# Optimization experiments

Measured on AMD Instinct MI355X. Metric: run time of the kernel, lower is better.

The kernel has to match this reference:

```python
import jax, jax.numpy as jnp
import numpy as np

T, B, H, W, CIN = 20, 16, 128, 128, 2
CH, OUT = 64, 10
BETA, THR = 0.9, 1.0


def spike(u):
    # Heaviside fire (surrogate grad only matters in bwd module)
    return (u > 0.0).astype(u.dtype)


def setup_inputs() -> dict:
    key = jax.random.key(0)
    k0, k1, k2 = jax.random.split(key, 3)
    x_seq = jax.random.normal(k0, (T, B, H, W, CIN), jnp.float32)
    w_conv = jax.random.normal(k1, (3, 3, CIN, CH), jnp.float32) * (1.0 / np.sqrt(9 * CIN))
    b_conv = jnp.zeros((CH,), jnp.float32)
    w_head = jax.random.normal(k2, (CH, OUT), jnp.float32) * (1.0 / np.sqrt(CH))
    b_head = jnp.zeros((OUT,), jnp.float32)
    return {"x_seq": x_seq, "w_conv": w_conv, "b_conv": b_conv,
            "w_head": w_head, "b_head": b_head}


def reference(x_seq, w_conv, b_conv, w_head, b_head):
    # temporal frame differences: [T-1, B, H, W, CIN]
    flow = x_seq[1:] - x_seq[:-1]
    t, b, h, w, c = flow.shape
    # conv is carry-independent: batch it over (time*batch) in one call
    u = jax.lax.conv_general_dilated(
        flow.reshape(t * b, h, w, c), w_conv,
        window_strides=(1, 1), padding='SAME',
        dimension_numbers=('NHWC', 'HWIO', 'NHWC')) + b_conv
    u = u.reshape(t, b, h, w, CH)  # [T-1, B, H, W, CH]

    def step(V, u_t):
        # LIF: leaky integrate, fire, soft reset
        V = BETA * V + u_t
        s = spike(V - THR)
        V = V - s * THR
        y = jnp.mean(s, axis=(1, 2)) @ w_head + b_head  # [B, OUT]
        return V, (y, jnp.mean(s))

    V0 = jnp.zeros((b, h, w, CH), u.dtype)
    _, (logits_seq, sr_seq) = jax.lax.scan(step, V0, u)
    readout = jnp.mean(logits_seq, axis=0)  # 'mean' readout
    return readout, logits_seq, jnp.asarray([jnp.mean(sr_seq)])
```

## Files before the change

kernel.cpp:

```cpp
#include <hip/hip_runtime.h>
#include <hip/hip_bf16.h>

#define TT   20
#define TS   19
#define BB   16
#define HH   128
#define WW   128
#define CINN 2
#define CHN  64
#define NOUT 10
#define BETA 0.9f
#define INVB (1.0f / BETA)

#define NCHUNK 5
#define NPB    128
#define SR_IDX (BB*NOUT + TS*BB*NOUT)

#define PPD      132
#define ROWB     (PPD*4)
#define PROWS    129
#define PLANE_B  (PROWS*ROWB)
#define FRAME_B  (2*PLANE_B)
#define FLOW_B   ((size_t)BB*TS*FRAME_B)
#define SLACK_B  528
#define CNT_OFF4 ((size_t)(FLOW_B + SLACK_B) / 4)
#define CNT_B    ((size_t)BB*NCHUNK*NPB*CHN*4)
#define WS_NEED  (FLOW_B + SLACK_B + CNT_B)

#define LROW  20

typedef __attribute__((ext_vector_type(8))) short short8;
typedef __attribute__((ext_vector_type(4))) float float4v;
typedef __attribute__((ext_vector_type(4))) int   int4v;
typedef unsigned uint4v_t __attribute__((ext_vector_type(4)));
typedef uint4v_t __attribute__((aligned(4))) uint4vu;
typedef unsigned uint2v_t __attribute__((ext_vector_type(2)));
typedef uint2v_t __attribute__((aligned(4))) uint2vu;

__device__ __forceinline__ unsigned rne16(float f) {
    unsigned u = __float_as_uint(f);
    return (u + 0x7fffu + ((u >> 16) & 1u)) >> 16;
}
__device__ __forceinline__ float b2f(unsigned us) { return __uint_as_float(us << 16); }
__device__ __forceinline__ unsigned rndb(float f) {
    unsigned u = __float_as_uint(f);
    return u + 0x7fffu + ((u >> 16) & 1u);
}
__device__ __forceinline__ void pack2(float d0, float d1, unsigned &hi, unsigned &lo) {
    unsigned r0 = rndb(d0), r1 = rndb(d1);
    hi = __builtin_amdgcn_perm(r1, r0, 0x07060302u);
    float e0 = d0 - __uint_as_float(r0 & 0xffff0000u);
    float e1 = d1 - __uint_as_float(r1 & 0xffff0000u);
    lo = __builtin_amdgcn_perm(rndb(e1), rndb(e0), 0x07060302u);
}

__global__ __launch_bounds__(256) void flow_pack(const float* __restrict__ x,
                                                 unsigned* __restrict__ wsf) {
    const int bx  = blockIdx.x;
    const int b   = blockIdx.y;
    const int tid = threadIdx.x;
    const int row = (bx << 2) + (tid >> 6);
    const int p0  = (tid & 63) << 1;

    const int TSTR = BB * HH * WW / 2;
    const float4* xr = (const float4*)x + ((b * HH + row) * WW + p0) / 2;
    char* fb = (char*)wsf + (size_t)b * TS * FRAME_B;
    const unsigned off = (unsigned)(row * PPD + p0 + 1) * 4u;

    float4 cur = xr[0];
    float4 nxt = xr[TSTR];
    float ct = 1.f;
#pragma unroll 1
    for (int t = 0; t < TS; ++t) {
        float4 fut = nxt;
        if (t + 2 <= TS) fut = xr[(t + 2) * TSTR];
        float d0 = (nxt.x - cur.x) * ct, d1 = (nxt.y - cur.y) * ct;
        float d2 = (nxt.z - cur.z) * ct, d3 = (nxt.w - cur.w) * ct;
        unsigned h0, l0, h1, l1;
        pack2(d0, d1, h0, l0);
        pack2(d2, d3, h1, l1);
        uint2v_t hv = {h0, h1}, lv = {l0, l1};
        *(uint2vu*)(fb + off) = hv;
        *(uint2vu*)(fb + PLANE_B + off) = lv;
        if ((tid & 63) < 8) {
            int c  = tid & 7;
            int pl = c >> 2;
            int pp = (c & 3) == 0 ? 0 : 128 + (c & 3);
            *(unsigned*)(fb + pl * PLANE_B + (row * PPD + pp) * 4) = 0u;
        }
        if (bx == 0) {
            for (int d = tid; d < 2 * PPD; d += 256) {
                int pl = d >= PPD, pp = d - pl * PPD;
                *(unsigned*)(fb + pl * PLANE_B + (128 * PPD + pp) * 4) = 0u;
            }
        }
        cur = nxt; nxt = fut;
        fb += FRAME_B; ct *= INVB;
    }
    if (bx == 0 && b == 0 && tid < PPD)
        *((unsigned*)((char*)wsf + FLOW_B) + tid) = 0u;
}

__global__ __launch_bounds__(256, 3) void lif_fast(const char* __restrict__ flow,
                                                   const float* __restrict__ w_conv,
                                                   const float* __restrict__ b_conv,
                                                   int* __restrict__ cw,
                                                   float* __restrict__ out) {
    __shared__ int lds_cnt[NCHUNK][CHN];

    const int tid  = threadIdx.x;
    const int lane = tid & 63;
    const int wv   = __builtin_amdgcn_readfirstlane(tid >> 6);
    const int bx   = blockIdx.x;
    const int r0   = blockIdx.y << 1;
    const int bz   = blockIdx.z;
    const int q    = lane >> 4;
    const int col  = lane & 15;
    const int x0   = (bx << 6) + (wv << 4);
    const int qsh  = q << 3;

    if (bx == 0 && blockIdx.y == 0 && bz == 0) {
        if (tid < BB * NOUT) out[tid] = 0.f;
        else if (tid == BB * NOUT) out[SR_IDX] = 0.f;
    }
    if (tid < NCHUNK * CHN - 256) ((int*)lds_cnt)[256 + tid] = 0;
    ((int*)lds_cnt)[tid] = 0;
    __syncthreads();

    const int rq  = (q < 3) ? q : 0;
    const int yA0 = r0 - 1 + rq, yA1 = yA0 + 1;
    const int ym0 = ((unsigned)yA0 < (unsigned)HH) ? yA0 : 128;
    const int ym1 = ((unsigned)yA1 < (unsigned)HH) ? yA1 : 128;
    const unsigned offH0 = (unsigned)(ym0 * ROWB + (x0 + col) * 4);
    const unsigned offH1 = (unsigned)(ym1 * ROWB + (x0 + col) * 4);

    short8 Bh[4], Bl[4];
#pragma unroll
    for (int cg = 0; cg < 4; ++cg) {
        int hi_i[4] = {0, 0, 0, 0}, lo_i[4] = {0, 0, 0, 0};
        if (q < 3) {
#pragma unroll
            for (int j = 0; j < 6; ++j) {
                float w = w_conv[((q * 3 + (j >> 1)) * 2 + (j & 1)) * CHN + cg * 16 + col];
                unsigned hs = rne16(w);
                unsigned ls = rne16(w - b2f(hs));
                hi_i[j >> 1] |= (int)(hs << (16 * (j & 1)));
                lo_i[j >> 1] |= (int)(ls << (16 * (j & 1)));
            }
        }
        int4v hv = {hi_i[0], hi_i[1], hi_i[2], hi_i[3]};
        int4v lv = {lo_i[0], lo_i[1], lo_i[2], lo_i[3]};
        Bh[cg] = __builtin_bit_cast(short8, hv);
        Bl[cg] = __builtin_bit_cast(short8, lv);
    }

    float nb[4];
#pragma unroll
    for (int cg = 0; cg < 4; ++cg) nb[cg] = -b_conv[cg * 16 + col];

    float4v W0[4], W1[4];
#pragma unroll
    for (int cg = 0; cg < 4; ++cg) {
        W0[cg] = (float4v){0.f, 0.f, 0.f, 0.f};
        W1[cg] = (float4v){0.f, 0.f, 0.f, 0.f};
    }

    float ct = 1.0f, S = 1.0f;
    int pendA = 0, pendB = 0;
    unsigned cur = 0;

    const char* fp = flow + (size_t)bz * TS * FRAME_B;
    uint4vu eH0 = *(const uint4vu*)(fp + offH0);
    uint4vu eH1 = *(const uint4vu*)(fp + offH1);
    uint4vu eL0 = *(const uint4vu*)(fp + PLANE_B + offH0);
    uint4vu eL1 = *(const uint4vu*)(fp + PLANE_B + offH1);
    fp += FRAME_B;
    uint4vu oH0, oH1, oL0, oL1;

#define STEP(T_, CH0, CH1, CL0, CL1, NH0, NH1, NL0, NL1, DPOS, DODEF, DOFLUSH, CK, DOLOAD) do { \
    int cp1_ = 0, sh2_ = 0;                                                     \
    if (DODEF) { cp1_ = pendA + pendB; sh2_ = __shfl_xor(cp1_, 32); }           \
    if (DOLOAD) {                                                               \
        NH0 = *(const uint4vu*)(fp + offH0);                                    \
        NH1 = *(const uint4vu*)(fp + offH1);                                    \
        NL0 = *(const uint4vu*)(fp + PLANE_B + offH0);                          \
        NL1 = *(const uint4vu*)(fp + PLANE_B + offH1);                          \
        fp += FRAME_B;                                                          \
    }                                                                           \
    float ctn = ct * INVB;                                                      \
    short8 A0h = __builtin_bit_cast(short8, CH0);                               \
    short8 A1h = __builtin_bit_cast(short8, CH1);                               \
    short8 A0l = __builtin_bit_cast(short8, CL0);                               \
    short8 A1l = __builtin_bit_cast(short8, CL1);                               \
    __builtin_amdgcn_s_setprio(1);                                              \
    _Pragma("unroll")                                                           \
    for (int cg = 0; cg < 4; ++cg) {                                            \
        W0[cg] = __builtin_amdgcn_mfma_f32_16x16x32_bf16(A0h, Bh[cg], W0[cg], 0, 0, 0); \
        W1[cg] = __builtin_amdgcn_mfma_f32_16x16x32_bf16(A1h, Bh[cg], W1[cg], 0, 0, 0); \
    }                                                                           \
    _Pragma("unroll")                                                           \
    for (int cg = 0; cg < 4; ++cg) {                                            \
        W0[cg] = __builtin_amdgcn_mfma_f32_16x16x32_bf16(A0l, Bh[cg], W0[cg], 0, 0, 0); \
        W1[cg] = __builtin_amdgcn_mfma_f32_16x16x32_bf16(A1l, Bh[cg], W1[cg], 0, 0, 0); \
    }                                                                           \
    _Pragma("unroll")                                                           \
    for (int cg = 0; cg < 4; ++cg) {                                            \
        W0[cg] = __builtin_amdgcn_mfma_f32_16x16x32_bf16(A0h, Bl[cg], W0[cg], 0, 0, 0); \
        W1[cg] = __builtin_amdgcn_mfma_f32_16x16x32_bf16(A1h, Bl[cg], W1[cg], 0, 0, 0); \
    }                                                                           \
    __builtin_amdgcn_s_setprio(0);                                              \
    if (DODEF) {                                                                \
        unsigned cnt_ = ((unsigned)(cp1_ + sh2_) >> qsh) & 255u;                \
        cur |= cnt_ << (8 * (DPOS));                                            \
        if (DOFLUSH) { atomicAdd(&lds_cnt[CK][lane], (int)cur); cur = 0u; }     \
    }                                                                           \
    int cpack = 0;                                                              \
    _Pragma("unroll")                                                           \
    for (int cg = 0; cg < 4; ++cg) {                                            \
        float thr = fmaf(nb[cg], S, ct);                                        \
        float4v w0 = W0[cg], w1 = W1[cg];                                       \
        int c = 0;                                                              \
        _Pragma("unroll")                                                       \
        for (int r = 0; r < 4; ++r) {                                           \
            float v0 = w0[r]; bool s0 = v0 > thr;                               \
            w0[r] = s0 ? (v0 - ct) : v0; c += s0;                               \
            float v1 = w1[r]; bool s1 = v1 > thr;                               \
            w1[r] = s1 ? (v1 - ct) : v1; c += s1;                               \
        }                                                                       \
        W0[cg] = w0; W1[cg] = w1;                                               \
        cpack |= c << (8 * cg);                                                 \
    }                                                                           \
    pendA = cpack;                                                              \
    pendB = __shfl_xor(cpack, 16);                                              \
    ct = ctn; S += ctn;                                                         \
} while (0)

#pragma unroll 1
    for (int c = 0; c < 4; ++c) {
        STEP(4 * c + 0, eH0, eH1, eL0, eL1, oH0, oH1, oL0, oL1, 3, (c > 0), (c > 0), (c - 1), 1);
        STEP(4 * c + 1, oH0, oH1, oL0, oL1, eH0, eH1, eL0, eL1, 0, 1, 0, 0, 1);
        STEP(4 * c + 2, eH0, eH1, eL0, eL1, oH0, oH1, oL0, oL1, 1, 1, 0, 0, 1);
        STEP(4 * c + 3, oH0, oH1, oL0, oL1, eH0, eH1, eL0, eL1, 2, 1, 0, 0, 1);
    }
    STEP(16, eH0, eH1, eL0, eL1, oH0, oH1, oL0, oL1, 3, 1, 1, 3, 1);
    STEP(17, oH0, oH1, oL0, oL1, eH0, eH1, eL0, eL1, 0, 1, 0, 0, 1);
    STEP(18, eH0, eH1, eL0, eL1, oH0, oH1, oL0, oL1, 1, 1, 0, 0, 0);
#undef STEP

    {
        int cp1 = pendA + pendB;
        int cp2 = cp1 + __shfl_xor(cp1, 32);
        unsigned cnt = ((unsigned)cp2 >> qsh) & 255u;
        cur |= cnt << 16;
        atomicAdd(&lds_cnt[4][lane], (int)cur);
    }
    __syncthreads();

    {
        const int pb = (blockIdx.y << 1) | bx;
        const int k0 = tid >> 6, ch = tid & 63;
        cw[((bz * NCHUNK + k0) * NPB + pb) * CHN + ch] = lds_cnt[k0][ch];
        if (tid < CHN)
            cw[((bz * NCHUNK + 4) * NPB + pb) * CHN + tid] = lds_cnt[4][tid];
    }
}

__global__ __launch_bounds__(256, 4) void lif_main(const float* __restrict__ x,
                                                   const float* __restrict__ w_conv,
                                                   const float* __restrict__ b_conv,
                                                   int* __restrict__ ws,
                                                   float* __restrict__ out) {
    __shared__ unsigned lds[4][2][2][4 * LROW];
    __shared__ int lds_cnt[NCHUNK][CHN];

    const float2* xp2 = (const float2*)x;
    const int FRAME2  = BB * HH * WW;

    const int tid  = threadIdx.x;
    const int lane = tid & 63;
    const int wv   = __builtin_amdgcn_readfirstlane(tid >> 6);
    const int bx   = blockIdx.x;
    const int r0   = blockIdx.y << 1;
    const int bz   = blockIdx.z;
    const int q    = lane >> 4;
    const int col  = lane & 15;
    const int x0   = (bx << 6) + (wv << 4);
    const int qsh  = q << 3;

    if (bx == 0 && blockIdx.y == 0 && bz == 0) {
        if (tid < BB * NOUT) out[tid] = 0.f;
        else if (tid == BB * NOUT) out[SR_IDX] = 0.f;
    }
    if (tid < NCHUNK * CHN - 256) ((int*)lds_cnt)[256 + tid] = 0;
    ((int*)lds_cnt)[tid] = 0;
    __syncthreads();

    const int  row0 = lane / 18, dx0 = lane - row0 * 18;
    const int  y0s  = r0 - 1 + row0;
    const int  px0s = x0 - 1 + dx0;
    const bool val0 = ((unsigned)y0s < (unsigned)HH) && ((unsigned)px0s < (unsigned)WW);
    const int  off0 = val0 ? (y0s * WW + px0s) : 0;
    const int  ls0  = row0 * LROW + dx0;

    const bool act1 = (lane < 8);
    const int  y1s  = r0 + 2;
    const int  px1s = x0 - 1 + 10 + lane;
    const bool val1 = act1 && ((unsigned)y1s < (unsigned)HH) && ((unsigned)px1s < (unsigned)WW);
    const int  off1 = val1 ? (y1s * WW + px1s) : 0;
    const int  ls1  = 3 * LROW + 10 + lane;

    const int rq  = (q < 3) ? q : 0;
    const int rdb = rq * LROW + col;

    short8 Bh[4], Bl[4];
#pragma unroll
    for (int cg = 0; cg < 4; ++cg) {
        int hi_i[4] = {0, 0, 0, 0}, lo_i[4] = {0, 0, 0, 0};
        if (q < 3) {
#pragma unroll
            for (int j = 0; j < 6; ++j) {
                float w = w_conv[((q * 3 + (j >> 1)) * 2 + (j & 1)) * CHN + cg * 16 + col];
                unsigned hs = rne16(w);
                unsigned ls = rne16(w - b2f(hs));
                hi_i[j >> 1] |= (int)(hs << (16 * (j & 1)));
                lo_i[j >> 1] |= (int)(ls << (16 * (j & 1)));
            }
        }
        int4v hv = {hi_i[0], hi_i[1], hi_i[2], hi_i[3]};
        int4v lv = {lo_i[0], lo_i[1], lo_i[2], lo_i[3]};
        Bh[cg] = __builtin_bit_cast(short8, hv);
        Bl[cg] = __builtin_bit_cast(short8, lv);
    }

    float nb[4];
#pragma unroll
    for (int cg = 0; cg < 4; ++cg) nb[cg] = -b_conv[cg * 16 + col];

    float4v W0[4], W1[4];
#pragma unroll
    for (int cg = 0; cg < 4; ++cg) {
        W0[cg] = (float4v){0.f, 0.f, 0.f, 0.f};
        W1[cg] = (float4v){0.f, 0.f, 0.f, 0.f};
    }

    float ct = 1.0f, S = 1.0f;
    int pendA = 0, pendB = 0;
    unsigned cur = 0;

    float2 ra_0 = {0.f, 0.f}, rb_0 = {0.f, 0.f}, rc_0 = {0.f, 0.f};
    float2 ra_1 = {0.f, 0.f}, rb_1 = {0.f, 0.f}, rc_1 = {0.f, 0.f};
    const float2* xb = xp2 + bz * HH * WW;
    if (val0) { rb_0 = xb[off0]; ra_0 = xb[FRAME2 + off0]; rc_0 = xb[2 * FRAME2 + off0]; }
    if (val1) { rb_1 = xb[off1]; ra_1 = xb[FRAME2 + off1]; rc_1 = xb[2 * FRAME2 + off1]; }
    {
        unsigned* hiW = &lds[wv][0][0][0];
        unsigned* loW = &lds[wv][0][1][0];
        {
            float d0 = (ra_0.x - rb_0.x), d1 = (ra_0.y - rb_0.y);
            unsigned hw, lw; pack2(d0, d1, hw, lw);
            hiW[ls0] = hw; loW[ls0] = lw;
        }
        if (act1) {
            float d0 = (ra_1.x - rb_1.x), d1 = (ra_1.y - rb_1.y);
            unsigned hw, lw; pack2(d0, d1, hw, lw);
            hiW[ls1] = hw; loW[ls1] = lw;
        }
        rb_0 = ra_0; ra_0 = rc_0;
        rb_1 = ra_1; ra_1 = rc_1;
        if (val0) rc_0 = xb[3 * FRAME2 + off0];
        if (val1) rc_1 = xb[3 * FRAME2 + off1];
    }
    const float2* xn = xb + 4 * FRAME2;

#define STEP(T_, CURB, NXTB, DPOS, DODEF, DOFLUSH, CK, DOSTAGE, DOPREF) do {    \
    const unsigned* hiR = &lds[wv][CURB][0][0] + rdb;                           \
    const unsigned* loR = &lds[wv][CURB][1][0] + rdb;                           \
    unsigned h0 = hiR[0], h1 = hiR[1], h2 = hiR[2];                             \
    unsigned h3 = hiR[LROW], h4 = hiR[LROW + 1], h5 = hiR[LROW + 2];            \
    unsigned l0 = loR[0], l1 = loR[1], l2 = loR[2];                             \
    unsigned l3 = loR[LROW], l4 = loR[LROW + 1], l5 = loR[LROW + 2];            \
    int cp1_ = 0, sh2_ = 0;                                                     \
    if (DODEF) { cp1_ = pendA + pendB; sh2_ = __shfl_xor(cp1_, 32); }           \
    float ctn = ct * INVB;                                                      \
    if (DOSTAGE) {                                                              \
        unsigned* hiW = &lds[wv][NXTB][0][0];                                   \
        unsigned* loW = &lds[wv][NXTB][1][0];                                   \
        {                                                                       \
            float d0 = (ra_0.x - rb_0.x) * ctn;                                 \
            float d1 = (ra_0.y - rb_0.y) * ctn;                                 \
            unsigned hw, lw; pack2(d0, d1, hw, lw);                             \
            hiW[ls0] = hw; loW[ls0] = lw;                                       \
        }                                                                       \
        if (act1) {                                                             \
            float d0 = (ra_1.x - rb_1.x) * ctn;                                 \
            float d1 = (ra_1.y - rb_1.y) * ctn;                                 \
            unsigned hw, lw; pack2(d0, d1, hw, lw);                             \
            hiW[ls1] = hw; loW[ls1] = lw;                                       \
        }                                                                       \
        rb_0 = ra_0; ra_0 = rc_0;                                               \
        rb_1 = ra_1; ra_1 = rc_1;                                               \
        if (DOPREF) {                                                           \
            if (val0) rc_0 = xn[off0];                                          \
            if (val1) rc_1 = xn[off1];                                          \
            xn += FRAME2;                                                       \
        }                                                                       \
    }                                                                           \
    int4v a0h = {(int)h0, (int)h1, (int)h2, (int)h0};                           \
    int4v a0l = {(int)l0, (int)l1, (int)l2, (int)l0};                           \
    int4v a1h = {(int)h3, (int)h4, (int)h5, (int)h3};                           \
    int4v a1l = {(int)l3, (int)l4, (int)l5, (int)l3};                           \
    short8 A0h = __builtin_bit_cast(short8, a0h);                               \
    short8 A0l = __builtin_bit_cast(short8, a0l);                               \
    short8 A1h = __builtin_bit_cast(short8, a1h);                               \
    short8 A1l = __builtin_bit_cast(short8, a1l);                               \
    __builtin_amdgcn_s_setprio(1);                                              \
    _Pragma("unroll")                                                           \
    for (int cg = 0; cg < 4; ++cg) {                                            \
        W0[cg] = __builtin_amdgcn_mfma_f32_16x16x32_bf16(A0h, Bh[cg], W0[cg], 0, 0, 0); \
        W1[cg] = __builtin_amdgcn_mfma_f32_16x16x32_bf16(A1h, Bh[cg], W1[cg], 0, 0, 0); \
    }                                                                           \
    _Pragma("unroll")                                                           \
    for (int cg = 0; cg < 4; ++cg) {                                            \
        W0[cg] = __builtin_amdgcn_mfma_f32_16x16x32_bf16(A0l, Bh[cg], W0[cg], 0, 0, 0); \
        W1[cg] = __builtin_amdgcn_mfma_f32_16x16x32_bf16(A1l, Bh[cg], W1[cg], 0, 0, 0); \
    }                                                                           \
    _Pragma("unroll")                                                           \
    for (int cg = 0; cg < 4; ++cg) {                                            \
        W0[cg] = __builtin_amdgcn_mfma_f32_16x16x32_bf16(A0h, Bl[cg], W0[cg], 0, 0, 0); \
        W1[cg] = __builtin_amdgcn_mfma_f32_16x16x32_bf16(A1h, Bl[cg], W1[cg], 0, 0, 0); \
    }                                                                           \
    __builtin_amdgcn_s_setprio(0);                                              \
    if (DODEF) {                                                                \
        unsigned cnt_ = ((unsigned)(cp1_ + sh2_) >> qsh) & 255u;                \
        cur |= cnt_ << (8 * (DPOS));                                            \
        if (DOFLUSH) { atomicAdd(&lds_cnt[CK][lane], (int)cur); cur = 0u; }     \
    }                                                                           \
    int cpack = 0;                                                              \
    _Pragma("unroll")                                                           \
    for (int cg = 0; cg < 4; ++cg) {                                            \
        float thr = fmaf(nb[cg], S, ct);                                        \
        float4v w0 = W0[cg], w1 = W1[cg];                                       \
        int c = 0;                                                              \
        _Pragma("unroll")                                                       \
        for (int r = 0; r < 4; ++r) {                                           \
            float v0 = w0[r]; bool s0 = v0 > thr;                               \
            w0[r] = s0 ? (v0 - ct) : v0; c += s0;                               \
            float v1 = w1[r]; bool s1 = v1 > thr;                               \
            w1[r] = s1 ? (v1 - ct) : v1; c += s1;                               \
        }                                                                       \
        W0[cg] = w0; W1[cg] = w1;                                               \
        cpack |= c << (8 * cg);                                                 \
    }                                                                           \
    pendA = cpack;                                                              \
    pendB = __shfl_xor(cpack, 16);                                              \
    ct = ctn; S += ctn;                                                         \
} while (0)

#pragma unroll 1
    for (int c = 0; c < 4; ++c) {
        STEP(4 * c + 0, 0, 1, 3, (c > 0), (c > 0), (c - 1), 1, 1);
        STEP(4 * c + 1, 1, 0, 0, 1, 0, 0, 1, 1);
        STEP(4 * c + 2, 0, 1, 1, 1, 0, 0, 1, 1);
        STEP(4 * c + 3, 1, 0, 2, 1, 0, 0, 1, 1);
    }
    STEP(16, 0, 1, 3, 1, 1, 3, 1, 0);
    STEP(17, 1, 0, 0, 1, 0, 0, 1, 0);
    STEP(18, 0, 1, 1, 1, 0, 0, 0, 0);
#undef STEP

    {
        int cp1 = pendA + pendB;
        int cp2 = cp1 + __shfl_xor(cp1, 32);
        unsigned cnt = ((unsigned)cp2 >> qsh) & 255u;
        cur |= cnt << 16;
        atomicAdd(&lds_cnt[4][lane], (int)cur);
    }
    __syncthreads();

    {
        const int pb = (blockIdx.y << 1) | bx;
        const int k0 = tid >> 6, ch = tid & 63;
        ws[((bz * NCHUNK + k0) * NPB + pb) * CHN + ch] = lds_cnt[k0][ch];
        if (tid < CHN)
            ws[((bz * NCHUNK + 4) * NPB + pb) * CHN + tid] = lds_cnt[4][tid];
    }
}

__global__ __launch_bounds__(64) void head_kernel(const int* __restrict__ cw,
                                                  const float* __restrict__ w_head,
                                                  const float* __restrict__ b_head,
                                                  float* __restrict__ out) {
    const int t = blockIdx.x, b = blockIdx.y, ch = threadIdx.x;
    const int k = t >> 2, sh = (t & 3) << 3;
    const int* base = cw + ((b * NCHUNK + k) * NPB) * CHN + ch;

    int cnt = 0;
#pragma unroll 8
    for (int p = 0; p < NPB; ++p) cnt += (base[p * CHN] >> sh) & 255;

    const float s = (float)cnt * (1.f / (HH * WW));
    float acc[NOUT];
#pragma unroll
    for (int o = 0; o < NOUT; ++o) acc[o] = s * w_head[ch * NOUT + o];
    float tt = (float)cnt;
#pragma unroll
    for (int off = 32; off > 0; off >>= 1) {
#pragma unroll
        for (int o = 0; o < NOUT; ++o) acc[o] += __shfl_down(acc[o], off);
        tt += __shfl_down(tt, off);
    }
    if (ch == 0) {
#pragma unroll
        for (int o = 0; o < NOUT; ++o) {
            float lg = acc[o] + b_head[o];
            out[BB * NOUT + (t * BB + b) * NOUT + o] = lg;
            atomicAdd(&out[b * NOUT + o], lg * (1.f / TS));
        }
        atomicAdd(&out[SR_IDX], tt * (1.f / ((float)TS * BB * HH * WW * CHN)));
    }
}

extern "C" void kernel_launch(void* const* d_in, const int* in_sizes, int n_in,
                              void* d_out, int out_size, void* d_ws, size_t ws_size,
                              hipStream_t stream) {
    (void)in_sizes; (void)n_in; (void)out_size;
    const float* x      = (const float*)d_in[0];
    const float* w_conv = (const float*)d_in[1];
    const float* b_conv = (const float*)d_in[2];
    const float* w_head = (const float*)d_in[3];
    const float* b_head = (const float*)d_in[4];
    float* out = (float*)d_out;

    if (ws_size >= WS_NEED) {
        unsigned* wsf = (unsigned*)d_ws;
        int* cw = (int*)d_ws + CNT_OFF4;
        flow_pack<<<dim3(32, BB), 256, 0, stream>>>(x, wsf);
        lif_fast<<<dim3(2, HH / 2, BB), 256, 0, stream>>>((const char*)d_ws, w_conv, b_conv, cw, out);
        head_kernel<<<dim3(TS, BB), 64, 0, stream>>>(cw, w_head, b_head, out);
    } else {
        int* cw = (int*)d_ws;
        lif_main<<<dim3(2, HH / 2, BB), 256, 0, stream>>>(x, w_conv, b_conv, cw, out);
        head_kernel<<<dim3(TS, BB), 64, 0, stream>>>(cw, w_head, b_head, out);
    }
}
```

Measured before the change: 167.4 us.

## Switch LIF conv MFMA from 16x16x32 to 32x32x16 tiles and raise occupancy

Result: slower. 171.8 us (+2.7%).

```diff
diff --git a/kernel.cpp b/kernel.cpp
--- a/kernel.cpp
+++ b/kernel.cpp
@@ -31,6 +31,7 @@
 
 typedef __attribute__((ext_vector_type(8))) short short8;
 typedef __attribute__((ext_vector_type(4))) float float4v;
+typedef __attribute__((ext_vector_type(16))) float floatv16;
 typedef __attribute__((ext_vector_type(4))) int   int4v;
 typedef unsigned uint4v_t __attribute__((ext_vector_type(4)));
 typedef uint4v_t __attribute__((aligned(4))) uint4vu;
@@ -101,7 +102,7 @@
         *((unsigned*)((char*)wsf + FLOW_B) + tid) = 0u;
 }
 
-__global__ __launch_bounds__(256, 3) void lif_fast(const char* __restrict__ flow,
+__global__ __launch_bounds__(256, 4) void lif_fast(const char* __restrict__ flow,
                                                    const float* __restrict__ w_conv,
                                                    const float* __restrict__ b_conv,
                                                    int* __restrict__ cw,
@@ -114,10 +115,9 @@
     const int bx   = blockIdx.x;
     const int r0   = blockIdx.y << 1;
     const int bz   = blockIdx.z;
-    const int q    = lane >> 4;
-    const int col  = lane & 15;
+    const int h    = lane >> 5;
+    const int colB = lane & 31;
     const int x0   = (bx << 6) + (wv << 4);
-    const int qsh  = q << 3;
 
     if (bx == 0 && blockIdx.y == 0 && bz == 0) {
         if (tid < BB * NOUT) out[tid] = 0.f;
@@ -127,131 +127,125 @@
     ((int*)lds_cnt)[tid] = 0;
     __syncthreads();
 
-    const int rq  = (q < 3) ? q : 0;
-    const int yA0 = r0 - 1 + rq, yA1 = yA0 + 1;
-    const int ym0 = ((unsigned)yA0 < (unsigned)HH) ? yA0 : 128;
-    const int ym1 = ((unsigned)yA1 < (unsigned)HH) ? yA1 : 128;
-    const unsigned offH0 = (unsigned)(ym0 * ROWB + (x0 + col) * 4);
-    const unsigned offH1 = (unsigned)(ym1 * ROWB + (x0 + col) * 4);
-
-    short8 Bh[4], Bl[4];
-#pragma unroll
-    for (int cg = 0; cg < 4; ++cg) {
-        int hi_i[4] = {0, 0, 0, 0}, lo_i[4] = {0, 0, 0, 0};
-        if (q < 3) {
-#pragma unroll
-            for (int j = 0; j < 6; ++j) {
-                float w = w_conv[((q * 3 + (j >> 1)) * 2 + (j & 1)) * CHN + cg * 16 + col];
-                unsigned hs = rne16(w);
-                unsigned ls = rne16(w - b2f(hs));
-                hi_i[j >> 1] |= (int)(hs << (16 * (j & 1)));
-                lo_i[j >> 1] |= (int)(ls << (16 * (j & 1)));
+    const int rimg = r0 + ((lane >> 4) & 1);
+    const int xpx  = x0 + (lane & 15);
+    const int ya   = rimg - 1 + h;
+    const int yb   = rimg + 1;
+    const int yam  = ((unsigned)ya < (unsigned)HH) ? ya : 128;
+    const int ybm  = ((unsigned)yb < (unsigned)HH) ? yb : 128;
+    const unsigned offQ0 = (unsigned)(yam * ROWB + xpx * 4);
+    const unsigned offQ1 = (unsigned)(ybm * ROWB + xpx * 4);
+
+    short8 Bh[2][2], Bl[2][2];
+#pragma unroll
+    for (int t = 0; t < 2; ++t) {
+#pragma unroll
+        for (int m = 0; m < 2; ++m) {
+            const int q = 2 * m + h;
+            int hi_i[4] = {0, 0, 0, 0}, lo_i[4] = {0, 0, 0, 0};
+            if (q < 3) {
+#pragma unroll
+                for (int e = 0; e < 6; ++e) {
+                    float w = w_conv[((q * 3 + (e >> 1)) * 2 + (e & 1)) * CHN + t * 32 + colB];
+                    unsigned hs = rne16(w);
+                    unsigned ls = rne16(w - b2f(hs));
+                    hi_i[e >> 1] |= (int)(hs << (16 * (e & 1)));
+                    lo_i[e >> 1] |= (int)(ls << (16 * (e & 1)));
+                }
             }
-        }
-        int4v hv = {hi_i[0], hi_i[1], hi_i[2], hi_i[3]};
-        int4v lv = {lo_i[0], lo_i[1], lo_i[2], lo_i[3]};
-        Bh[cg] = __builtin_bit_cast(short8, hv);
-        Bl[cg] = __builtin_bit_cast(short8, lv);
-    }
-
-    float nb[4];
-#pragma unroll
-    for (int cg = 0; cg < 4; ++cg) nb[cg] = -b_conv[cg * 16 + col];
-
-    float4v W0[4], W1[4];
-#pragma unroll
-    for (int cg = 0; cg < 4; ++cg) {
-        W0[cg] = (float4v){0.f, 0.f, 0.f, 0.f};
-        W1[cg] = (float4v){0.f, 0.f, 0.f, 0.f};
-    }
+            int4v hv = {hi_i[0], hi_i[1], hi_i[2], hi_i[3]};
+            int4v lv = {lo_i[0], lo_i[1], lo_i[2], lo_i[3]};
+            Bh[t][m] = __builtin_bit_cast(short8, hv);
+            Bl[t][m] = __builtin_bit_cast(short8, lv);
+        }
+    }
+
+    const float nb0 = -b_conv[colB];
+    const float nb1 = -b_conv[32 + colB];
+
+    floatv16 W0 = {0.f,0.f,0.f,0.f,0.f,0.f,0.f,0.f,0.f,0.f,0.f,0.f,0.f,0.f,0.f,0.f};
+    floatv16 W1 = {0.f,0.f,0.f,0.f,0.f,0.f,0.f,0.f,0.f,0.f,0.f,0.f,0.f,0.f,0.f,0.f};
 
     float ct = 1.0f, S = 1.0f;
-    int pendA = 0, pendB = 0;
+    int pend = 0;
     unsigned cur = 0;
 
     const char* fp = flow + (size_t)bz * TS * FRAME_B;
-    uint4vu eH0 = *(const uint4vu*)(fp + offH0);
-    uint4vu eH1 = *(const uint4vu*)(fp + offH1);
-    uint4vu eL0 = *(const uint4vu*)(fp + PLANE_B + offH0);
-    uint4vu eL1 = *(const uint4vu*)(fp + PLANE_B + offH1);
+    uint4vu eQ0h = *(const uint4vu*)(fp + offQ0);
+    uint4vu eQ1h = *(const uint4vu*)(fp + offQ1);
+    uint4vu eQ0l = *(const uint4vu*)(fp + PLANE_B + offQ0);
+    uint4vu eQ1l = *(const uint4vu*)(fp + PLANE_B + offQ1);
     fp += FRAME_B;
-    uint4vu oH0, oH1, oL0, oL1;
-
-#define STEP(T_, CH0, CH1, CL0, CL1, NH0, NH1, NL0, NL1, DPOS, DODEF, DOFLUSH, CK, DOLOAD) do { \
-    int cp1_ = 0, sh2_ = 0;                                                     \
-    if (DODEF) { cp1_ = pendA + pendB; sh2_ = __shfl_xor(cp1_, 32); }           \
+    uint4vu oQ0h, oQ1h, oQ0l, oQ1l;
+
+#define MFMA32 __builtin_amdgcn_mfma_f32_32x32x16_bf16
+
+#define STEP(T_, CQ0H, CQ1H, CQ0L, CQ1L, NQ0H, NQ1H, NQ0L, NQ1L, DPOS, DODEF, DOFLUSH, CK, DOLOAD) do { \
+    int sh_ = 0;                                                                \
+    if (DODEF) sh_ = __shfl_xor(pend, 32);                                      \
     if (DOLOAD) {                                                               \
-        NH0 = *(const uint4vu*)(fp + offH0);                                    \
-        NH1 = *(const uint4vu*)(fp + offH1);                                    \
-        NL0 = *(const uint4vu*)(fp + PLANE_B + offH0);                          \
-        NL1 = *(const uint4vu*)(fp + PLANE_B + offH1);                          \
+        NQ0H = *(const uint4vu*)(fp + offQ0);                                   \
+        NQ1H = *(const uint4vu*)(fp + offQ1);                                   \
+        NQ0L = *(const uint4vu*)(fp + PLANE_B + offQ0);                         \
+        NQ1L = *(const uint4vu*)(fp + PLANE_B + offQ1);                         \
         fp += FRAME_B;                                                          \
     }                                                                           \
     float ctn = ct * INVB;                                                      \
-    short8 A0h = __builtin_bit_cast(short8, CH0);                               \
-    short8 A1h = __builtin_bit_cast(short8, CH1);                               \
-    short8 A0l = __builtin_bit_cast(short8, CL0);                               \
-    short8 A1l = __builtin_bit_cast(short8, CL1);                               \
+    short8 A0h = __builtin_bit_cast(short8, CQ0H);                              \
+    short8 A1h = __builtin_bit_cast(short8, CQ1H);                              \
+    short8 A0l = __builtin_bit_cast(short8, CQ0L);                              \
+    short8 A1l = __builtin_bit_cast(short8, CQ1L);                              \
     __builtin_amdgcn_s_setprio(1);                                              \
-    _Pragma("unroll")                                                           \
-    for (int cg = 0; cg < 4; ++cg) {                                            \
-        W0[cg] = __builtin_amdgcn_mfma_f32_16x16x32_bf16(A0h, Bh[cg], W0[cg], 0, 0, 0); \
-        W1[cg] = __builtin_amdgcn_mfma_f32_16x16x32_bf16(A1h, Bh[cg], W1[cg], 0, 0, 0); \
-    }                                                                           \
-    _Pragma("unroll")                                                           \
-    for (int cg = 0; cg < 4; ++cg) {                                            \
-        W0[cg] = __builtin_amdgcn_mfma_f32_16x16x32_bf16(A0l, Bh[cg], W0[cg], 0, 0, 0); \
-        W1[cg] = __builtin_amdgcn_mfma_f32_16x16x32_bf16(A1l, Bh[cg], W1[cg], 0, 0, 0); \
-    }                                                                           \
-    _Pragma("unroll")                                                           \
-    for (int cg = 0; cg < 4; ++cg) {                                            \
-        W0[cg] = __builtin_amdgcn_mfma_f32_16x16x32_bf16(A0h, Bl[cg], W0[cg], 0, 0, 0); \
-        W1[cg] = __builtin_amdgcn_mfma_f32_16x16x32_bf16(A1h, Bl[cg], W1[cg], 0, 0, 0); \
-    }                                                                           \
+    W0 = MFMA32(A0h, Bh[0][0], W0, 0, 0, 0);                                    \
+    W1 = MFMA32(A0h, Bh[1][0], W1, 0, 0, 0);                                    \
+    W0 = MFMA32(A1h, Bh[0][1], W0, 0, 0, 0);                                    \
+    W1 = MFMA32(A1h, Bh[1][1], W1, 0, 0, 0);                                    \
+    W0 = MFMA32(A0l, Bh[0][0], W0, 0, 0, 0);                                    \
+    W1 = MFMA32(A0l, Bh[1][0], W1, 0, 0, 0);                                    \
+    W0 = MFMA32(A1l, Bh[0][1], W0, 0, 0, 0);                                    \
+    W1 = MFMA32(A1l, Bh[1][1], W1, 0, 0, 0);                                    \
+    W0 = MFMA32(A0h, Bl[0][0], W0, 0, 0, 0);                                    \
+    W1 = MFMA32(A0h, Bl[1][0], W1, 0, 0, 0);                                    \
+    W0 = MFMA32(A1h, Bl[0][1], W0, 0, 0, 0);                                    \
+    W1 = MFMA32(A1h, Bl[1][1], W1, 0, 0, 0);                                    \
     __builtin_amdgcn_s_setprio(0);                                              \
     if (DODEF) {                                                                \
-        unsigned cnt_ = ((unsigned)(cp1_ + sh2_) >> qsh) & 255u;                \
-        cur |= cnt_ << (8 * (DPOS));                                            \
+        unsigned tot_ = (unsigned)(pend + sh_);                                 \
+        unsigned mych = (tot_ >> (h << 3)) & 255u;                              \
+        cur |= mych << (8 * (DPOS));                                            \
         if (DOFLUSH) { atomicAdd(&lds_cnt[CK][lane], (int)cur); cur = 0u; }     \
     }                                                                           \
-    int cpack = 0;                                                              \
+    float thr0 = fmaf(nb0, S, ct);                                              \
+    float thr1 = fmaf(nb1, S, ct);                                              \
+    int c0 = 0, c1 = 0;                                                         \
     _Pragma("unroll")                                                           \
-    for (int cg = 0; cg < 4; ++cg) {                                            \
-        float thr = fmaf(nb[cg], S, ct);                                        \
-        float4v w0 = W0[cg], w1 = W1[cg];                                       \
-        int c = 0;                                                              \
-        _Pragma("unroll")                                                       \
-        for (int r = 0; r < 4; ++r) {                                           \
-            float v0 = w0[r]; bool s0 = v0 > thr;                               \
-            w0[r] = s0 ? (v0 - ct) : v0; c += s0;                               \
-            float v1 = w1[r]; bool s1 = v1 > thr;                               \
-            w1[r] = s1 ? (v1 - ct) : v1; c += s1;                               \
-        }                                                                       \
-        W0[cg] = w0; W1[cg] = w1;                                               \
-        cpack |= c << (8 * cg);                                                 \
-    }                                                                           \
-    pendA = cpack;                                                              \
-    pendB = __shfl_xor(cpack, 16);                                              \
+    for (int r = 0; r < 16; ++r) {                                              \
+        float v0 = W0[r]; bool s0 = v0 > thr0;                                  \
+        W0[r] = s0 ? (v0 - ct) : v0; c0 += s0;                                  \
+        float v1 = W1[r]; bool s1 = v1 > thr1;                                  \
+        W1[r] = s1 ? (v1 - ct) : v1; c1 += s1;                                  \
+    }                                                                           \
+    pend = c0 | (c1 << 8);                                                      \
     ct = ctn; S += ctn;                                                         \
 } while (0)
 
 #pragma unroll 1
     for (int c = 0; c < 4; ++c) {
-        STEP(4 * c + 0, eH0, eH1, eL0, eL1, oH0, oH1, oL0, oL1, 3, (c > 0), (c > 0), (c - 1), 1);
-        STEP(4 * c + 1, oH0, oH1, oL0, oL1, eH0, eH1, eL0, eL1, 0, 1, 0, 0, 1);
-        STEP(4 * c + 2, eH0, eH1, eL0, eL1, oH0, oH1, oL0, oL1, 1, 1, 0, 0, 1);
-        STEP(4 * c + 3, oH0, oH1, oL0, oL1, eH0, eH1, eL0, eL1, 2, 1, 0, 0, 1);
-    }
-    STEP(16, eH0, eH1, eL0, eL1, oH0, oH1, oL0, oL1, 3, 1, 1, 3, 1);
-    STEP(17, oH0, oH1, oL0, oL1, eH0, eH1, eL0, eL1, 0, 1, 0, 0, 1);
-    STEP(18, eH0, eH1, eL0, eL1, oH0, oH1, oL0, oL1, 1, 1, 0, 0, 0);
+        STEP(4 * c + 0, eQ0h, eQ1h, eQ0l, eQ1l, oQ0h, oQ1h, oQ0l, oQ1l, 3, (c > 0), (c > 0), (c - 1), 1);
+        STEP(4 * c + 1, oQ0h, oQ1h, oQ0l, oQ1l, eQ0h, eQ1h, eQ0l, eQ1l, 0, 1, 0, 0, 1);
+        STEP(4 * c + 2, eQ0h, eQ1h, eQ0l, eQ1l, oQ0h, oQ1h, oQ0l, oQ1l, 1, 1, 0, 0, 1);
+        STEP(4 * c + 3, oQ0h, oQ1h, oQ0l, oQ1l, eQ0h, eQ1h, eQ0l, eQ1l, 2, 1, 0, 0, 1);
+    }
+    STEP(16, eQ0h, eQ1h, eQ0l, eQ1l, oQ0h, oQ1h, oQ0l, oQ1l, 3, 1, 1, 3, 1);
+    STEP(17, oQ0h, oQ1h, oQ0l, oQ1l, eQ0h, eQ1h, eQ0l, eQ1l, 0, 1, 0, 0, 1);
+    STEP(18, eQ0h, eQ1h, eQ0l, eQ1l, oQ0h, oQ1h, oQ0l, oQ1l, 1, 1, 0, 0, 0);
 #undef STEP
+#undef MFMA32
 
     {
-        int cp1 = pendA + pendB;
-        int cp2 = cp1 + __shfl_xor(cp1, 32);
-        unsigned cnt = ((unsigned)cp2 >> qsh) & 255u;
-        cur |= cnt << 16;
+        int sh = __shfl_xor(pend, 32);
+        unsigned mych = ((unsigned)(pend + sh) >> (h << 3)) & 255u;
+        cur |= mych << 16;
         atomicAdd(&lds_cnt[4][lane], (int)cur);
     }
     __syncthreads();
```
